# Kernel optimization log

Hardware: AMD Instinct MI355X
Metric: run time of the kernel (lower is better)

Reference implementation:

```python
import jax, jax.numpy as jnp
import numpy as np

B, N, NH, F = 4, 4096, 16, 8      # batch, grid cells, input points per cell, raw features
D, FF, H, PE = 256, 1024, 8, 32   # model_dim, ff_dim, n_heads, pos_emb_dim
NG, NI = 8192, 65536              # grid table size, input-point table size
SEQ = 4                           # 4 ** seq_level
HD = D // H


def layer_norm(x, g, b, eps=1e-5):
    mu = jnp.mean(x, axis=-1, keepdims=True)
    var = jnp.mean(jnp.square(x - mu), axis=-1, keepdims=True)
    return (x - mu) * jax.lax.rsqrt(var + eps) * g + b


def setup_inputs() -> dict:
    key = jax.random.key(0)
    ks = jax.random.split(key, 20)
    inp = {}
    inp["x"] = jax.random.normal(ks[0], (B, N, NH, F), jnp.float32)
    inp["grid_level_indices"] = jax.random.randint(ks[1], (B, N), 0, NG)
    inp["drop_mask"] = jax.random.bernoulli(ks[2], 0.1, (B, N))
    # buffers
    inp["input_mapping"] = jax.random.randint(ks[3], (NG, NH), 0, NI)
    inp["in_range"] = jax.random.bernoulli(ks[4], 0.95, (NG, NH))
    inp["input_coordinates"] = jax.random.uniform(ks[5], (2, NI), jnp.float32, -3.14, 3.14)
    inp["grid_coords"] = jax.random.uniform(ks[6], (2, NG), jnp.float32, -3.14, 3.14)
    # params
    inp["W_in"] = jax.random.normal(ks[7], (F, D), jnp.float32) * 0.05
    inp["b_in"] = jnp.zeros((D,), jnp.float32)
    inp["W_pe"] = jax.random.normal(ks[8], (2, PE), jnp.float32) * 0.2
    inp["W_bias"] = jax.random.normal(ks[9], (PE, H), jnp.float32) * 0.1
    inp["W_v"] = jax.random.normal(ks[10], (D, D), jnp.float32) * 0.02
    inp["W_o"] = jax.random.normal(ks[11], (D, D), jnp.float32) * 0.02
    inp["W1"] = jax.random.normal(ks[12], (D, FF), jnp.float32) * 0.02
    inp["W2"] = jax.random.normal(ks[13], (FF, D), jnp.float32) * 0.02
    inp["g1"] = jnp.ones((D,), jnp.float32)
    inp["b1"] = jnp.zeros((D,), jnp.float32)
    inp["g2"] = jnp.ones((D,), jnp.float32)
    inp["b2"] = jnp.zeros((D,), jnp.float32)
    return inp


def reference(x, grid_level_indices, drop_mask, input_mapping, in_range,
              input_coordinates, grid_coords, W_in, b_in, W_pe, W_bias,
              W_v, W_o, W1, W2, g1, b1, g2, b2):
    b, n, nh, _ = x.shape
    nq = n // SEQ
    K = SEQ * nh  # keys per group

    # input_layer.input_mlp: Linear + SiLU
    x = jax.nn.silu(x @ W_in + b_in)                       # [b,n,nh,D]

    # relative positions (polar): grid-cell coords vs gathered input-point coords
    gseq = grid_level_indices.reshape(b, nq, SEQ)
    idx = input_mapping[gseq]                              # [b,nq,4,nh]
    lon1 = grid_coords[0][gseq][..., None, None]           # [b,nq,4,1,1]
    lat1 = grid_coords[1][gseq][..., None, None]
    lon2 = input_coordinates[0][idx][:, :, None]           # [b,nq,1,4,nh]
    lat2 = input_coordinates[1][idx][:, :, None]
    dlon, dlat = lon2 - lon1, lat2 - lat1                  # [b,nq,4,4,nh]
    dist = jnp.sqrt(dlon * dlon + dlat * dlat + 1e-12)
    ang = jnp.arctan2(dlat, dlon)
    pos1 = dist.reshape(b, nq, SEQ, K)
    pos2 = ang.reshape(b, nq, SEQ, K)

    # mask: out-of-range OR dropped, broadcast across the 4 query cells
    m = (~in_range[grid_level_indices]) | drop_mask[:, :, None]  # [b,n,nh]
    m = m.reshape(b, nq, SEQ, nh)
    mask = jnp.broadcast_to(m[:, :, None], (b, nq, SEQ, SEQ, nh)).reshape(b, nq, SEQ, K)

    xs = x.reshape(b, nq, K, D)                            # kv tokens per group

    # positional bias -> attention scores (qkv_bias=False path: bias-only scores)
    pe = jax.nn.silu(jnp.stack([pos1, pos2], -1) @ W_pe)   # [b,nq,4,K,PE]
    bias = pe @ W_bias                                     # [b,nq,4,K,H]
    scores = jnp.moveaxis(bias, -1, 2)                     # [b,nq,H,4,K]
    scores = jnp.where(mask[:, :, None], -1e9, scores)
    att = jax.nn.softmax(scores, axis=-1)

    vh = (xs @ W_v).reshape(b, nq, K, H, HD)
    out = jnp.einsum('bqhtk,bqkhd->bqthd', att, vh).reshape(b, nq, SEQ, D)
    out = out @ W_o                                        # [b,nq,4,D]

    # nha_layer tail (q_res=False, dropout=0)
    h = layer_norm(out, g1, b1)
    h = layer_norm(h + jax.nn.silu(h @ W1) @ W2, g2, b2)
    return h.reshape(b, n, D)
```

## Files before the change

### kernel.cpp

```cpp
#include <hip/hip_runtime.h>

#define B_   4
#define N_   4096
#define NH_  16
#define F_   8
#define D_   256
#define FF_  1024
#define H_   8
#define PE_  32
#define NG_  8192
#define NI_  65536
#define NQ_  1024

typedef short short8 __attribute__((ext_vector_type(8)));
typedef short short4v __attribute__((ext_vector_type(4)));
typedef float f32x4 __attribute__((ext_vector_type(4)));

union U8 { short8 s8; uint4 u4; };

__device__ __forceinline__ float silu_f(float v) {
  return v * __builtin_amdgcn_rcpf(1.f + __expf(-v));
}
__device__ __forceinline__ unsigned short f2bf(float f) {
  unsigned int x = __float_as_uint(f);
  unsigned int r = (x + 0x7fffu + ((x >> 16) & 1u)) >> 16;
  return (unsigned short)r;
}
__device__ __forceinline__ unsigned int cvt_pk(float a, float b) {
  unsigned int r;
  asm("v_cvt_pk_bf16_f32 %0, %1, %2" : "=v"(r) : "v"(a), "v"(b));
  return r;
}
__device__ __forceinline__ unsigned short f2bf1(float v) {
  return (unsigned short)cvt_pk(v, v);
}
__device__ __forceinline__ float bf2f(unsigned short h) {
  return __uint_as_float(((unsigned int)h) << 16);
}

__device__ __forceinline__ int detect_layout(const unsigned int* w) {
  unsigned b1 = 0, b0 = 0;
#pragma unroll
  for (int i = 0; i < 64; ++i) {
    unsigned v = w[i];
    b1 |= v & 0x0000FF00u;
    b0 |= v & 0x000000FFu;
  }
  return b1 ? 0 : (b0 ? 1 : 2);
}
__device__ __forceinline__ int read_bool(const void* p, int i, int lay) {
  if (lay == 0) return ((const unsigned char*)p)[i] != 0;
  if (lay == 1) return ((const int*)p)[i] != 0;
  return ((const float*)p)[i] != 0.0f;
}

#define WOP_OFF 0
#define W1P_OFF 65536
#define W2P_OFF (65536 + 262144)
#define WVP_OFF (65536 + 262144 + 262144)
#define WIP_OFF (65536 + 262144 + 262144 + 65536)
#define WBP_OFF (WIP_OFF + 8192)
#define WS_TAIL ((65536 + 262144 + 262144) * 2)
#define WS_FULL ((WBP_OFF + 512) * 2)

__global__ __launch_bounds__(256) void k_pack(
    const float* __restrict__ Wo, const float* __restrict__ W1,
    const float* __restrict__ W2, const float* __restrict__ Wv,
    const float* __restrict__ Wi, const float* __restrict__ Wb,
    short* __restrict__ ws)
{
  int t = blockIdx.x * 256 + threadIdx.x;
  if (t < 8192) {
    int g = t & 3, n = (t >> 2) & 255, kk = t >> 10;
    int k0 = kk * 32 + g * 8;
    short8 v;
#pragma unroll
    for (int j = 0; j < 8; ++j) v[j] = (short)f2bf(Wo[(k0 + j) * 256 + n]);
    *(short8*)(ws + WOP_OFF + t * 8) = v;
  } else if (t < 40960) {
    int u = t - 8192;
    int g = u & 3, n = (u >> 2) & 1023, kk = u >> 12;
    int k0 = kk * 32 + g * 8;
    short8 v;
#pragma unroll
    for (int j = 0; j < 8; ++j) v[j] = (short)f2bf(W1[(k0 + j) * 1024 + n]);
    *(short8*)(ws + W1P_OFF + u * 8) = v;
  } else if (t < 73728) {
    int u = t - 40960;
    int g = u & 3, n = (u >> 2) & 255, kk = u >> 10;
    int k0 = kk * 32 + g * 8;
    short8 v;
#pragma unroll
    for (int j = 0; j < 8; ++j) v[j] = (short)f2bf(W2[(k0 + j) * 256 + n]);
    *(short8*)(ws + W2P_OFF + u * 8) = v;
  } else if (t < 81920) {
    int u = t - 73728;
    int g = u & 3, n = (u >> 2) & 255, kk = u >> 10;
    int k0 = kk * 32 + g * 8;
    short8 v;
#pragma unroll
    for (int j = 0; j < 8; ++j) v[j] = (short)f2bf(Wv[(k0 + j) * 256 + n]);
    *(short8*)(ws + WVP_OFF + u * 8) = v;
  } else if (t < 82944) {
    int u = t - 81920;
    int g = u & 3, n = u >> 2;
    short8 v;
#pragma unroll
    for (int j = 0; j < 8; ++j) {
      int k = g * 8 + j;
      v[j] = (k < 8) ? (short)f2bf(Wi[k * 256 + n]) : (short)0;
    }
    *(short8*)(ws + WIP_OFF + (n * 4 + g) * 8) = v;
  } else if (t < 83008) {
    int u = t - 82944;
    int g = u & 3, col = u >> 2;
    short8 v;
#pragma unroll
    for (int j = 0; j < 8; ++j) {
      int p = g * 8 + j;
      v[j] = (col < 8) ? (short)f2bf(Wb[p * 8 + col]) : (short)0;
    }
    *(short8*)(ws + WBP_OFF + (col * 4 + g) * 8) = v;
  }
}

#define OFF_XST   0
#define OFF_ATTB  32768
#define OFF_XL    36864
#define OFF_DIST  36864
#define OFF_ANG   37888
#define OFF_KLON  38912
#define OFF_KLAT  39168
#define OFF_KMSK  39424
#define OFF_GLON  39680
#define OFF_GLAT  39696
#define OFF_GIDX  39712
#define OFF_DROP  39728

__global__ __launch_bounds__(256) void k_attn_mfma(
    const float* __restrict__ x, const int* __restrict__ gli,
    const void* __restrict__ drop, const int* __restrict__ imap,
    const void* __restrict__ inr, const float* __restrict__ icoord,
    const float* __restrict__ gcoord, const float* __restrict__ W_pe,
    const float* __restrict__ b_in, const short* __restrict__ WiP,
    const short* __restrict__ WbP, const short* __restrict__ WvP,
    float* __restrict__ out)
{
  __shared__ __align__(16) char sm[39744];
  float* xl = (float*)(sm + OFF_XL);
  float* distl = (float*)(sm + OFF_DIST);
  float* angl = (float*)(sm + OFF_ANG);
  float* klon = (float*)(sm + OFF_KLON);
  float* klat = (float*)(sm + OFF_KLAT);
  int* kmask = (int*)(sm + OFF_KMSK);
  float* glon = (float*)(sm + OFF_GLON);
  float* glat = (float*)(sm + OFF_GLAT);
  int* gidx = (int*)(sm + OFF_GIDX);
  int* dropf = (int*)(sm + OFF_DROP);

  const int grp = blockIdx.x;
  const int b = grp >> 10;
  const int q = grp & (NQ_ - 1);
  const int tid = threadIdx.x;
  const int w = tid >> 6;
  const int l15 = tid & 15;
  const int g = (tid & 63) >> 4;
  const int swz = (l15 & 7) << 4;

  const int lay = detect_layout((const unsigned int*)inr);

  if (tid < 4) {
    int gg = gli[b * N_ + q * 4 + tid];
    gidx[tid] = gg;
    glon[tid] = gcoord[gg];
    glat[tid] = gcoord[NG_ + gg];
    dropf[tid] = read_bool(drop, b * N_ + q * 4 + tid, lay);
  }
  const float* xb = x + (size_t)(b * N_ + q * 4) * (NH_ * F_);
  xl[tid] = xb[tid];
  xl[tid + 256] = xb[tid + 256];
  __syncthreads();

  if (tid < 64) {
    int s = tid >> 4;
    int gg = gidx[s];
    int id = imap[gg * NH_ + (tid & 15)];
    klon[tid] = icoord[id];
    klat[tid] = icoord[NI_ + id];
    kmask[tid] = (read_bool(inr, gg * NH_ + (tid & 15), lay) == 0) | dropf[s];
  }

  {
    short8 a = {0, 0, 0, 0, 0, 0, 0, 0};
    if (g == 0) {
      const float4* xlf = (const float4*)xl;
      float4 xa = xlf[(w * 16 + l15) * 2];
      float4 xc = xlf[(w * 16 + l15) * 2 + 1];
      U8 u;
      u.u4.x = cvt_pk(xa.x, xa.y);
      u.u4.y = cvt_pk(xa.z, xa.w);
      u.u4.z = cvt_pk(xc.x, xc.y);
      u.u4.w = cvt_pk(xc.z, xc.w);
      a = u.s8;
    }
    const int k0 = w * 16 + g * 4;
#pragma unroll
    for (int nf = 0; nf < 16; ++nf) {
      short8 bv = *(const short8*)(WiP + ((nf * 16 + l15) * 4 + g) * 8);
      f32x4 accM = {0.f, 0.f, 0.f, 0.f};
      accM = __builtin_amdgcn_mfma_f32_16x16x32_bf16(a, bv, accM, 0, 0, 0);
      int d = nf * 16 + l15;
      float bn = b_in[d];
      uint2 pv;
      pv.x = cvt_pk(silu_f(accM[0] + bn), silu_f(accM[1] + bn));
      pv.y = cvt_pk(silu_f(accM[2] + bn), silu_f(accM[3] + bn));
      *(uint2*)(sm + ((d * 128 + k0 * 2) ^ ((d & 7) << 4))) = pv;
    }
  }
  __syncthreads();

  {
    const int t = tid >> 6, k = tid & 63;
    float dlon = klon[k] - glon[t];
    float dlat = klat[k] - glat[t];
    distl[tid] = sqrtf(dlon * dlon + dlat * dlat + 1e-12f);
    angl[tid] = atan2f(dlat, dlon);
  }
  __syncthreads();

  {
    float wpe0[8], wpe1[8];
    {
      const float4* wp = (const float4*)W_pe;
      float4 w0a = wp[g * 2], w0b = wp[g * 2 + 1];
      float4 w1a = wp[8 + g * 2], w1b = wp[8 + g * 2 + 1];
      wpe0[0] = w0a.x; wpe0[1] = w0a.y; wpe0[2] = w0a.z; wpe0[3] = w0a.w;
      wpe0[4] = w0b.x; wpe0[5] = w0b.y; wpe0[6] = w0b.z; wpe0[7] = w0b.w;
      wpe1[0] = w1a.x; wpe1[1] = w1a.y; wpe1[2] = w1a.z; wpe1[3] = w1a.w;
      wpe1[4] = w1b.x; wpe1[5] = w1b.y; wpe1[6] = w1b.z; wpe1[7] = w1b.w;
    }
    short8 wb = *(const short8*)(WbP + (l15 * 4 + g) * 8);
    f32x4 accS[4];
#pragma unroll
    for (int i = 0; i < 4; ++i) {
      int row = (w * 4 + i) * 16 + l15;
      float dd = distl[row];
      float aa = angl[row];
      float pe[8];
#pragma unroll
      for (int j = 0; j < 8; ++j)
        pe[j] = silu_f(fmaf(dd, wpe0[j], aa * wpe1[j]));
      U8 pu;
      pu.u4.x = cvt_pk(pe[0], pe[1]);
      pu.u4.y = cvt_pk(pe[2], pe[3]);
      pu.u4.z = cvt_pk(pe[4], pe[5]);
      pu.u4.w = cvt_pk(pe[6], pe[7]);
      f32x4 z = {0.f, 0.f, 0.f, 0.f};
      accS[i] = __builtin_amdgcn_mfma_f32_16x16x32_bf16(pu.s8, wb, z, 0, 0, 0);
    }
    float sv[16];
    float mx = -1e30f;
#pragma unroll
    for (int i = 0; i < 4; ++i)
#pragma unroll
      for (int r = 0; r < 4; ++r) {
        int k = i * 16 + g * 4 + r;
        float s = kmask[k] ? -1e9f : accS[i][r];
        sv[i * 4 + r] = s;
        mx = fmaxf(mx, s);
      }
    mx = fmaxf(mx, __shfl_xor(mx, 16));
    mx = fmaxf(mx, __shfl_xor(mx, 32));
    float sum = 0.f;
#pragma unroll
    for (int u = 0; u < 16; ++u) { sv[u] = __expf(sv[u] - mx); sum += sv[u]; }
    sum += __shfl_xor(sum, 16);
    sum += __shfl_xor(sum, 32);
    float inv = __builtin_amdgcn_rcpf(sum);
    if (l15 < 8) {
      int row = l15 * 4 + w;
      int rs = (row & 7) << 4;
#pragma unroll
      for (int i = 0; i < 4; ++i) {
        uint2 pv;
        pv.x = cvt_pk(sv[i * 4 + 0] * inv, sv[i * 4 + 1] * inv);
        pv.y = cvt_pk(sv[i * 4 + 2] * inv, sv[i * 4 + 3] * inv);
        *(uint2*)(sm + OFF_ATTB + ((row * 128 + (i * 16 + g * 4) * 2) ^ rs)) = pv;
      }
    }
  }
  __syncthreads();

  f32x4 accY[2][4];
  {
    f32x4 z = {0.f, 0.f, 0.f, 0.f};
#pragma unroll
    for (int mi = 0; mi < 2; ++mi)
#pragma unroll
      for (int ni = 0; ni < 4; ++ni) accY[mi][ni] = z;
  }
#pragma unroll
  for (int kk = 0; kk < 2; ++kk) {
    short8 a0 = *(const short8*)(sm + OFF_ATTB + ((l15 * 128 + kk * 64 + g * 16) ^ swz));
    short8 a1 = *(const short8*)(sm + OFF_ATTB + (((16 + l15) * 128 + kk * 64 + g * 16) ^ swz));
    short8 bf[4];
#pragma unroll
    for (int ni = 0; ni < 4; ++ni)
      bf[ni] = *(const short8*)(sm +
          (((w * 64 + ni * 16 + l15) * 128 + kk * 64 + g * 16) ^ swz));
#pragma unroll
    for (int ni = 0; ni < 4; ++ni) {
      accY[0][ni] = __builtin_amdgcn_mfma_f32_16x16x32_bf16(a0, bf[ni], accY[0][ni], 0, 0, 0);
      accY[1][ni] = __builtin_amdgcn_mfma_f32_16x16x32_bf16(a1, bf[ni], accY[1][ni], 0, 0, 0);
    }
  }
  __syncthreads();

#pragma unroll
  for (int mi = 0; mi < 2; ++mi)
#pragma unroll
    for (int ni = 0; ni < 4; ++ni)
#pragma unroll
      for (int r = 0; r < 4; ++r) {
        int row = mi * 16 + g * 4 + r;
        int col = w * 64 + ni * 16 + l15;
        *(unsigned short*)(sm + ((row * 512 + col * 2) ^ ((row & 7) << 4))) =
            f2bf1(accY[mi][ni][r]);
      }
  __syncthreads();

  {
    const int mf = w >> 1;
    f32x4 accV[4];
    {
      f32x4 z = {0.f, 0.f, 0.f, 0.f};
#pragma unroll
      for (int ni = 0; ni < 4; ++ni) accV[ni] = z;
    }
#pragma unroll
    for (int kk = 0; kk < 8; ++kk) {
      short8 a = *(const short8*)(sm +
          (((mf * 16 + l15) * 512 + kk * 64 + g * 16) ^ swz));
#pragma unroll
      for (int ni = 0; ni < 4; ++ni) {
        int col = w * 64 + ni * 16 + l15;
        short8 bv = *(const short8*)(WvP + ((size_t)(kk * 256 + col)) * 32 + g * 8);
        accV[ni] = __builtin_amdgcn_mfma_f32_16x16x32_bf16(a, bv, accV[ni], 0, 0, 0);
      }
    }
    float* outl = (float*)(sm + 16384);
    const int gb = (w & 1) * 2;
#pragma unroll
    for (int ni = 0; ni < 4; ++ni) {
      if (g == gb + (ni >> 1)) {
#pragma unroll
        for (int r = 0; r < 4; ++r)
          outl[r * 256 + w * 64 + ni * 16 + l15] = accV[ni][r];
      }
    }
  }
  __syncthreads();

  {
    const float* outl = (const float*)(sm + 16384);
    float* ob = out + (size_t)grp * (4 * D_);
#pragma unroll
    for (int t = 0; t < 4; ++t) ob[t * 256 + tid] = outl[t * 256 + tid];
  }
}

__global__ __launch_bounds__(256) void k_attn_valu(
    const float* __restrict__ x, const int* __restrict__ gli,
    const void* __restrict__ drop, const int* __restrict__ imap,
    const void* __restrict__ inr, const float* __restrict__ icoord,
    const float* __restrict__ gcoord, const float* __restrict__ W_in,
    const float* __restrict__ b_in, const float* __restrict__ W_pe,
    const float* __restrict__ W_bias, const float* __restrict__ W_v,
    float* __restrict__ out)
{
  __shared__ __align__(16) float xl[512];
  __shared__ float glon[4], glat[4];
  __shared__ int gidx[4], dropf[4];
  __shared__ float klon[64], klat[64];
  __shared__ int kmask[64];
  __shared__ __align__(16) unsigned short xs[64 * D_];
  __shared__ __align__(16) float att[32 * 64];
  __shared__ __align__(16) float yl[4 * 8 * 260];

  const int grp = blockIdx.x;
  const int b = grp >> 10;
  const int q = grp & (NQ_ - 1);
  const int tid = threadIdx.x;
  const int lay = detect_layout((const unsigned int*)inr);

  if (tid < 4) {
    int g = gli[b * N_ + q * 4 + tid];
    gidx[tid] = g;
    glon[tid] = gcoord[g];
    glat[tid] = gcoord[NG_ + g];
    dropf[tid] = read_bool(drop, b * N_ + q * 4 + tid, lay);
  }
  const float* xb = x + (size_t)(b * N_ + q * 4) * (NH_ * F_);
  xl[tid] = xb[tid];
  xl[tid + 256] = xb[tid + 256];
  __syncthreads();

  if (tid < 64) {
    int s = tid >> 4;
    int g = gidx[s];
    int id = imap[g * NH_ + (tid & 15)];
    klon[tid] = icoord[id];
    klat[tid] = icoord[NI_ + id];
    kmask[tid] = (read_bool(inr, g * NH_ + (tid & 15), lay) == 0) | dropf[s];
  }
  {
    float w[8];
#pragma unroll
    for (int c = 0; c < 8; ++c) w[c] = W_in[c * D_ + tid];
    float bi = b_in[tid];
#pragma unroll 4
    for (int k = 0; k < 64; ++k) {
      float v = bi;
#pragma unroll
      for (int c = 0; c < 8; ++c) v = fmaf(xl[k * 8 + c], w[c], v);
      xs[k * D_ + tid] = f2bf(silu_f(v));
    }
  }
  __syncthreads();
  {
    const int t = tid >> 6, k = tid & 63;
    float dlon = klon[k] - glon[t];
    float dlat = klat[k] - glat[t];
    float dist = sqrtf(dlon * dlon + dlat * dlat + 1e-12f);
    float ang = atan2f(dlat, dlon);
    float bias[8];
#pragma unroll
    for (int h = 0; h < 8; ++h) bias[h] = 0.f;
#pragma unroll
    for (int p = 0; p < 32; ++p) {
      float pv = silu_f(fmaf(dist, W_pe[p], ang * W_pe[32 + p]));
#pragma unroll
      for (int h = 0; h < 8; ++h) bias[h] = fmaf(pv, W_bias[p * 8 + h], bias[h]);
    }
    const bool mk = (kmask[k] != 0);
#pragma unroll
    for (int h = 0; h < 8; ++h)
      att[(h * 4 + t) * 64 + k] = mk ? -1e9f : bias[h];
  }
  __syncthreads();
  {
    const int row = tid >> 3, l8 = tid & 7;
    float sv[8];
    float mx = -1e30f;
#pragma unroll
    for (int i = 0; i < 8; ++i) { sv[i] = att[row * 64 + l8 + i * 8]; mx = fmaxf(mx, sv[i]); }
#pragma unroll
    for (int off = 1; off < 8; off <<= 1) mx = fmaxf(mx, __shfl_xor(mx, off, 8));
    float sm = 0.f;
#pragma unroll
    for (int i = 0; i < 8; ++i) { sv[i] = __expf(sv[i] - mx); sm += sv[i]; }
#pragma unroll
    for (int off = 1; off < 8; off <<= 1) sm += __shfl_xor(sm, off, 8);
    float inv = 1.f / sm;
#pragma unroll
    for (int i = 0; i < 8; ++i) att[row * 64 + l8 + i * 8] = sv[i] * inv;
  }
  __syncthreads();
  {
    float acc[32];
#pragma unroll
    for (int r = 0; r < 32; ++r) acc[r] = 0.f;
    for (int k4 = 0; k4 < 64; k4 += 4) {
      float xv0 = bf2f(xs[(k4 + 0) * D_ + tid]);
      float xv1 = bf2f(xs[(k4 + 1) * D_ + tid]);
      float xv2 = bf2f(xs[(k4 + 2) * D_ + tid]);
      float xv3 = bf2f(xs[(k4 + 3) * D_ + tid]);
#pragma unroll
      for (int r = 0; r < 32; ++r) {
        float4 a = *(const float4*)&att[r * 64 + k4];
        acc[r] = fmaf(a.x, xv0, acc[r]);
        acc[r] = fmaf(a.y, xv1, acc[r]);
        acc[r] = fmaf(a.z, xv2, acc[r]);
        acc[r] = fmaf(a.w, xv3, acc[r]);
      }
    }
#pragma unroll
    for (int r = 0; r < 32; ++r)
      yl[(r & 3) * 2080 + (r >> 2) * 260 + tid] = acc[r];
  }
  __syncthreads();
  {
    const int h = tid >> 5;
    float o0 = 0.f, o1 = 0.f, o2 = 0.f, o3 = 0.f;
    for (int c = 0; c < 256; c += 4) {
      float w0 = W_v[(c + 0) * D_ + tid];
      float w1 = W_v[(c + 1) * D_ + tid];
      float w2 = W_v[(c + 2) * D_ + tid];
      float w3 = W_v[(c + 3) * D_ + tid];
      float4 y0 = *(const float4*)&yl[0 * 2080 + h * 260 + c];
      float4 y1 = *(const float4*)&yl[1 * 2080 + h * 260 + c];
      float4 y2 = *(const float4*)&yl[2 * 2080 + h * 260 + c];
      float4 y3 = *(const float4*)&yl[3 * 2080 + h * 260 + c];
      o0 = fmaf(y0.x, w0, o0); o0 = fmaf(y0.y, w1, o0); o0 = fmaf(y0.z, w2, o0); o0 = fmaf(y0.w, w3, o0);
      o1 = fmaf(y1.x, w0, o1); o1 = fmaf(y1.y, w1, o1); o1 = fmaf(y1.z, w2, o1); o1 = fmaf(y1.w, w3, o1);
      o2 = fmaf(y2.x, w0, o2); o2 = fmaf(y2.y, w1, o2); o2 = fmaf(y2.z, w2, o2); o2 = fmaf(y2.w, w3, o2);
      o3 = fmaf(y3.x, w0, o3); o3 = fmaf(y3.y, w1, o3); o3 = fmaf(y3.z, w2, o3); o3 = fmaf(y3.w, w3, o3);
    }
    float* ob = out + (size_t)grp * (4 * D_);
    ob[0 * D_ + tid] = o0;
    ob[1 * D_ + tid] = o1;
    ob[2 * D_ + tid] = o2;
    ob[3 * D_ + tid] = o3;
  }
}

template<int MI>
__device__ __forceinline__ void gemm_mfma(
    f32x4 acc[MI][4], const char* As, const short* Bp,
    int N, int kk0, int colbase, int l15, int g)
{
#pragma unroll
  for (int kk = 0; kk < 8; ++kk) {
    short8 a[MI], bv[4];
#pragma unroll
    for (int mi = 0; mi < MI; ++mi) {
      int row = mi * 16 + l15;
      int byte = (row * 512 + kk * 64 + g * 16) ^ ((row & 7) << 4);
      a[mi] = *(const short8*)(As + byte);
    }
#pragma unroll
    for (int ni = 0; ni < 4; ++ni) {
      int col = colbase + ni * 16 + l15;
      size_t off = ((size_t)(kk0 + kk) * N + col) * 32 + g * 8;
      bv[ni] = *(const short8*)(Bp + off);
    }
#pragma unroll
    for (int mi = 0; mi < MI; ++mi)
#pragma unroll
      for (int ni = 0; ni < 4; ++ni)
        acc[mi][ni] = __builtin_amdgcn_mfma_f32_16x16x32_bf16(
            a[mi], bv[ni], acc[mi][ni], 0, 0, 0);
  }
}

__global__ __launch_bounds__(256) void k_tail_mfma(
    const float* __restrict__ g1v, const float* __restrict__ b1v,
    const float* __restrict__ g2v, const float* __restrict__ b2v,
    const short* __restrict__ WoP, const short* __restrict__ W1P,
    const short* __restrict__ W2P, float* __restrict__ io)
{
  __shared__ __align__(16) unsigned short sA1[32 * 256];
  __shared__ __align__(16) unsigned short sU[32 * 256];
  __shared__ float sPs[4][32];
  __shared__ float sPss[4][32];

  const int tid = threadIdx.x;
  const int w = tid >> 6;
  const int l15 = tid & 15;
  const int g = (tid & 63) >> 4;
  float* base = io + (size_t)blockIdx.x * (32 * 256);

#pragma unroll
  for (int i = 0; i < 8; ++i) {
    int e = (tid + 256 * i) * 4;
    int row = e >> 8, c = e & 255;
    float4 v = *(const float4*)(base + e);
    uint2 pv;
    pv.x = cvt_pk(v.x, v.y);
    pv.y = cvt_pk(v.z, v.w);
    int byte = (row * 512 + c * 2) ^ ((row & 7) << 4);
    *(uint2*)((char*)sU + byte) = pv;
  }
  __syncthreads();

  f32x4 acc[2][4];
  {
    f32x4 z = {0.f, 0.f, 0.f, 0.f};
#pragma unroll
    for (int mi = 0; mi < 2; ++mi)
#pragma unroll
      for (int ni = 0; ni < 4; ++ni) acc[mi][ni] = z;
  }
  gemm_mfma<2>(acc, (const char*)sU, WoP, 256, 0, w * 64, l15, g);

#pragma unroll
  for (int mi = 0; mi < 2; ++mi)
#pragma unroll
    for (int r = 0; r < 4; ++r) {
      float a0 = acc[mi][0][r], a1 = acc[mi][1][r], a2 = acc[mi][2][r], a3 = acc[mi][3][r];
      float s = a0 + a1 + a2 + a3;
      float ss = a0 * a0 + a1 * a1 + a2 * a2 + a3 * a3;
#pragma unroll
      for (int off = 1; off < 16; off <<= 1) {
        s += __shfl_xor(s, off);
        ss += __shfl_xor(ss, off);
      }
      if (l15 == 0) {
        int row = 16 * mi + 4 * g + r;
        sPs[w][row] = s;
        sPss[w][row] = ss;
      }
    }
  __syncthreads();

  {
    float ga[4], bb[4];
#pragma unroll
    for (int ni = 0; ni < 4; ++ni) {
      int col = 64 * w + 16 * ni + l15;
      ga[ni] = g1v[col];
      bb[ni] = b1v[col];
    }
#pragma unroll
    for (int mi = 0; mi < 2; ++mi)
#pragma unroll
      for (int r = 0; r < 4; ++r) {
        int row = 16 * mi + 4 * g + r;
        float S = sPs[0][row] + sPs[1][row] + sPs[2][row] + sPs[3][row];
        float SS = sPss[0][row] + sPss[1][row] + sPss[2][row] + sPss[3][row];
        float mu = S * (1.f / 256.f);
        float rs = rsqrtf(SS * (1.f / 256.f) - mu * mu + 1e-5f);
#pragma unroll
        for (int ni = 0; ni < 4; ++ni) {
          int col = 64 * w + 16 * ni + l15;
          float val = (acc[mi][ni][r] - mu) * rs * ga[ni] + bb[ni];
          acc[mi][ni][r] = val;
          int byte = (row * 512 + col * 2) ^ ((row & 7) << 4);
          *(unsigned short*)((char*)sA1 + byte) = f2bf1(val);
        }
      }
  }
  __syncthreads();

  for (int p = 0; p < 4; ++p) {
    f32x4 acc2[2][4];
    {
      f32x4 z = {0.f, 0.f, 0.f, 0.f};
#pragma unroll
      for (int mi = 0; mi < 2; ++mi)
#pragma unroll
        for (int ni = 0; ni < 4; ++ni) acc2[mi][ni] = z;
    }
    gemm_mfma<2>(acc2, (const char*)sA1, W1P, 1024, 0, p * 256 + w * 64, l15, g);
#pragma unroll
    for (int mi = 0; mi < 2; ++mi)
#pragma unroll
      for (int ni = 0; ni < 4; ++ni)
#pragma unroll
        for (int r = 0; r < 4; ++r) {
          int row = 16 * mi + 4 * g + r;
          int col = 64 * w + 16 * ni + l15;
          int byte = (row * 512 + col * 2) ^ ((row & 7) << 4);
          *(unsigned short*)((char*)sU + byte) = f2bf1(silu_f(acc2[mi][ni][r]));
        }
    __syncthreads();
    gemm_mfma<2>(acc, (const char*)sU, W2P, 256, p * 8, w * 64, l15, g);
    __syncthreads();
  }

#pragma unroll
  for (int mi = 0; mi < 2; ++mi)
#pragma unroll
    for (int r = 0; r < 4; ++r) {
      float a0 = acc[mi][0][r], a1 = acc[mi][1][r], a2 = acc[mi][2][r], a3 = acc[mi][3][r];
      float s = a0 + a1 + a2 + a3;
      float ss = a0 * a0 + a1 * a1 + a2 * a2 + a3 * a3;
#pragma unroll
      for (int off = 1; off < 16; off <<= 1) {
        s += __shfl_xor(s, off);
        ss += __shfl_xor(ss, off);
      }
      if (l15 == 0) {
        int row = 16 * mi + 4 * g + r;
        sPs[w][row] = s;
        sPss[w][row] = ss;
      }
    }
  __syncthreads();

  {
    float ga[4], bb[4];
#pragma unroll
    for (int ni = 0; ni < 4; ++ni) {
      int col = 64 * w + 16 * ni + l15;
      ga[ni] = g2v[col];
      bb[ni] = b2v[col];
    }
#pragma unroll
    for (int mi = 0; mi < 2; ++mi)
#pragma unroll
      for (int r = 0; r < 4; ++r) {
        int row = 16 * mi + 4 * g + r;
        float S = sPs[0][row] + sPs[1][row] + sPs[2][row] + sPs[3][row];
        float SS = sPss[0][row] + sPss[1][row] + sPss[2][row] + sPss[3][row];
        float mu = S * (1.f / 256.f);
        float rs = rsqrtf(SS * (1.f / 256.f) - mu * mu + 1e-5f);
#pragma unroll
        for (int ni = 0; ni < 4; ++ni) {
          int col = 64 * w + 16 * ni + l15;
          base[row * 256 + col] = (acc[mi][ni][r] - mu) * rs * ga[ni] + bb[ni];
        }
      }
  }
}

__global__ __launch_bounds__(256) void k_tail(
    const float* __restrict__ Wo, const float* __restrict__ W1,
    const float* __restrict__ W2, const float* __restrict__ g1,
    const float* __restrict__ b1, const float* __restrict__ g2,
    const float* __restrict__ b2, float* __restrict__ io)
{
  __shared__ __align__(16) float rl[16 * 260];
  __shared__ __align__(16) float h1[16 * 260];
  __shared__ __align__(16) unsigned short u[16 * FF_];
  const int tid = threadIdx.x;
  float* base = io + (size_t)blockIdx.x * (16 * D_);

#pragma unroll
  for (int r = 0; r < 16; ++r) rl[r * 260 + tid] = base[r * D_ + tid];
  __syncthreads();
  {
    float acc[16];
#pragma unroll
    for (int r = 0; r < 16; ++r) acc[r] = 0.f;
    for (int c = 0; c < 256; c += 4) {
      float w0 = Wo[(c + 0) * D_ + tid], w1 = Wo[(c + 1) * D_ + tid];
      float w2 = Wo[(c + 2) * D_ + tid], w3 = Wo[(c + 3) * D_ + tid];
#pragma unroll
      for (int r = 0; r < 16; ++r) {
        float4 rv = *(const float4*)&rl[r * 260 + c];
        acc[r] = fmaf(rv.x, w0, acc[r]); acc[r] = fmaf(rv.y, w1, acc[r]);
        acc[r] = fmaf(rv.z, w2, acc[r]); acc[r] = fmaf(rv.w, w3, acc[r]);
      }
    }
#pragma unroll
    for (int r = 0; r < 16; ++r) h1[r * 260 + tid] = acc[r];
  }
  __syncthreads();
  {
    const int r = tid >> 4, l = tid & 15;
    float s = 0.f, ss = 0.f;
#pragma unroll
    for (int i = 0; i < 16; ++i) { float v = h1[r * 260 + l + i * 16]; s += v; ss += v * v; }
#pragma unroll
    for (int off = 1; off < 16; off <<= 1) { s += __shfl_xor(s, off, 16); ss += __shfl_xor(ss, off, 16); }
    float mu = s * (1.f / 256.f);
    float rs = rsqrtf(ss * (1.f / 256.f) - mu * mu + 1e-5f);
#pragma unroll
    for (int i = 0; i < 16; ++i) {
      int d = l + i * 16;
      h1[r * 260 + d] = (h1[r * 260 + d] - mu) * rs * g1[d] + b1[d];
    }
  }
  __syncthreads();
  for (int fo = 0; fo < 4; ++fo) {
    const int f = fo * 256 + tid;
    float a2[16];
#pragma unroll
    for (int r = 0; r < 16; ++r) a2[r] = 0.f;
    for (int c = 0; c < 256; c += 4) {
      float w0 = W1[(c + 0) * FF_ + f], w1 = W1[(c + 1) * FF_ + f];
      float w2 = W1[(c + 2) * FF_ + f], w3 = W1[(c + 3) * FF_ + f];
#pragma unroll
      for (int r = 0; r < 16; ++r) {
        float4 hv = *(const float4*)&h1[r * 260 + c];
        a2[r] = fmaf(hv.x, w0, a2[r]); a2[r] = fmaf(hv.y, w1, a2[r]);
        a2[r] = fmaf(hv.z, w2, a2[r]); a2[r] = fmaf(hv.w, w3, a2[r]);
      }
    }
#pragma unroll
    for (int r = 0; r < 16; ++r) u[r * FF_ + f] = f2bf(silu_f(a2[r]));
  }
  __syncthreads();
  {
    float a3[16];
#pragma unroll
    for (int r = 0; r < 16; ++r) a3[r] = h1[r * 260 + tid];
    for (int f = 0; f < FF_; f += 8) {
      float w[8];
#pragma unroll
      for (int i = 0; i < 8; ++i) w[i] = W2[(f + i) * D_ + tid];
#pragma unroll
      for (int r = 0; r < 16; ++r) {
        uint4 uv = *(const uint4*)&u[r * FF_ + f];
        a3[r] = fmaf(__uint_as_float(uv.x << 16), w[0], a3[r]);
        a3[r] = fmaf(__uint_as_float(uv.x & 0xffff0000u), w[1], a3[r]);
        a3[r] = fmaf(__uint_as_float(uv.y << 16), w[2], a3[r]);
        a3[r] = fmaf(__uint_as_float(uv.y & 0xffff0000u), w[3], a3[r]);
        a3[r] = fmaf(__uint_as_float(uv.z << 16), w[4], a3[r]);
        a3[r] = fmaf(__uint_as_float(uv.z & 0xffff0000u), w[5], a3[r]);
        a3[r] = fmaf(__uint_as_float(uv.w << 16), w[6], a3[r]);
        a3[r] = fmaf(__uint_as_float(uv.w & 0xffff0000u), w[7], a3[r]);
      }
    }
#pragma unroll
    for (int r = 0; r < 16; ++r) rl[r * 260 + tid] = a3[r];
  }
  __syncthreads();
  {
    const int r = tid >> 4, l = tid & 15;
    float s = 0.f, ss = 0.f;
#pragma unroll
    for (int i = 0; i < 16; ++i) { float v = rl[r * 260 + l + i * 16]; s += v; ss += v * v; }
#pragma unroll
    for (int off = 1; off < 16; off <<= 1) { s += __shfl_xor(s, off, 16); ss += __shfl_xor(ss, off, 16); }
    float mu = s * (1.f / 256.f);
    float rs = rsqrtf(ss * (1.f / 256.f) - mu * mu + 1e-5f);
#pragma unroll
    for (int i = 0; i < 16; ++i) {
      int d = l + i * 16;
      base[r * D_ + d] = (rl[r * 260 + d] - mu) * rs * g2[d] + b2[d];
    }
  }
}

extern "C" void kernel_launch(void* const* d_in, const int* in_sizes, int n_in,
                              void* d_out, int out_size, void* d_ws, size_t ws_size,
                              hipStream_t stream) {
  (void)in_sizes; (void)n_in; (void)out_size;
  const float* x = (const float*)d_in[0];
  const int* gli = (const int*)d_in[1];
  const void* drop = d_in[2];
  const int* imap = (const int*)d_in[3];
  const void* inr = d_in[4];
  const float* icoord = (const float*)d_in[5];
  const float* gcoord = (const float*)d_in[6];
  const float* W_in = (const float*)d_in[7];
  const float* b_in = (const float*)d_in[8];
  const float* W_pe = (const float*)d_in[9];
  const float* W_bias = (const float*)d_in[10];
  const float* W_v = (const float*)d_in[11];
  const float* W_o = (const float*)d_in[12];
  const float* W1 = (const float*)d_in[13];
  const float* W2 = (const float*)d_in[14];
  const float* g1 = (const float*)d_in[15];
  const float* b1 = (const float*)d_in[16];
  const float* g2 = (const float*)d_in[17];
  const float* b2 = (const float*)d_in[18];
  float* out = (float*)d_out;

  if (ws_size >= (size_t)WS_FULL) {
    short* ws = (short*)d_ws;
    k_pack<<<dim3(325), dim3(256), 0, stream>>>(W_o, W1, W2, W_v, W_in, W_bias, ws);
    k_attn_mfma<<<dim3(B_ * NQ_), dim3(256), 0, stream>>>(
        x, gli, drop, imap, inr, icoord, gcoord, W_pe, b_in,
        ws + WIP_OFF, ws + WBP_OFF, ws + WVP_OFF, out);
    k_tail_mfma<<<dim3((B_ * N_) / 32), dim3(256), 0, stream>>>(
        g1, b1, g2, b2, ws + WOP_OFF, ws + W1P_OFF, ws + W2P_OFF, out);
  } else if (ws_size >= (size_t)WS_TAIL) {
    short* ws = (short*)d_ws;
    k_pack<<<dim3(325), dim3(256), 0, stream>>>(W_o, W1, W2, W_v, W_in, W_bias, ws);
    k_attn_valu<<<dim3(B_ * NQ_), dim3(256), 0, stream>>>(
        x, gli, drop, imap, inr, icoord, gcoord, W_in, b_in, W_pe, W_bias, W_v, out);
    k_tail_mfma<<<dim3((B_ * N_) / 32), dim3(256), 0, stream>>>(
        g1, b1, g2, b2, ws + WOP_OFF, ws + W1P_OFF, ws + W2P_OFF, out);
  } else {
    k_attn_valu<<<dim3(B_ * NQ_), dim3(256), 0, stream>>>(
        x, gli, drop, imap, inr, icoord, gcoord, W_in, b_in, W_pe, W_bias, W_v, out);
    k_tail<<<dim3((B_ * N_) / 16), dim3(256), 0, stream>>>(
        W_o, W1, W2, g1, b1, g2, b2, out);
  }
}
```

Baseline: 115.7 us.

## Precompute byte masks, pass bf16 intermediate rows, drop x LDS staging

The pack kernel now converts the drop and in_range masks into byte arrays once, so the attention kernel no longer runs layout detection or reads the booleans per block. When the workspace is large enough, the attention kernel writes its output as bf16 rows into the workspace, and the tail kernel reads them directly instead of reading fp32 and converting, which halves that intermediate traffic. The x staging through LDS and one barrier are removed, with x loaded straight from global memory. In exchange the pack kernel launches more blocks, the fast path needs a larger workspace, and the k_attn_valu fallback now runs with pack blocks that never fill the masks.

Result: faster. 112.1 us (-3.1%).

```diff
diff --git a/kernel.cpp b/kernel.cpp
--- a/kernel.cpp
+++ b/kernel.cpp
@@ -13,7 +13,6 @@
 #define NQ_  1024
 
 typedef short short8 __attribute__((ext_vector_type(8)));
-typedef short short4v __attribute__((ext_vector_type(4)));
 typedef float f32x4 __attribute__((ext_vector_type(4)));
 
 union U8 { short8 s8; uint4 u4; };
@@ -60,13 +59,19 @@
 #define WVP_OFF (65536 + 262144 + 262144)
 #define WIP_OFF (65536 + 262144 + 262144 + 65536)
 #define WBP_OFF (WIP_OFF + 8192)
+#define WS_BASE_B ((WBP_OFF + 512) * 2)
+#define DRP8_B  WS_BASE_B
+#define INR8_B  (WS_BASE_B + 16384)
+#define WS_MASKS_END (INR8_B + 131072)
+#define ROWS_B  WS_MASKS_END
+#define WS_ROWS_END (ROWS_B + 16384 * 256 * 2)
 #define WS_TAIL ((65536 + 262144 + 262144) * 2)
-#define WS_FULL ((WBP_OFF + 512) * 2)
 
 __global__ __launch_bounds__(256) void k_pack(
     const float* __restrict__ Wo, const float* __restrict__ W1,
     const float* __restrict__ W2, const float* __restrict__ Wv,
     const float* __restrict__ Wi, const float* __restrict__ Wb,
+    const void* __restrict__ drop, const void* __restrict__ inr,
     short* __restrict__ ws)
 {
   int t = blockIdx.x * 256 + threadIdx.x;
@@ -121,12 +126,23 @@
       v[j] = (col < 8) ? (short)f2bf(Wb[p * 8 + col]) : (short)0;
     }
     *(short8*)(ws + WBP_OFF + (col * 4 + g) * 8) = v;
+  } else if (t >= 83200) {
+    int lay = detect_layout((const unsigned int*)inr);
+    int t2 = t - 83200;
+    char* wsb = (char*)ws;
+    if (t2 < B_ * N_) {
+      ((unsigned char*)(wsb + DRP8_B))[t2] =
+          (unsigned char)read_bool(drop, t2, lay);
+    } else if (t2 < B_ * N_ + NG_ * NH_) {
+      int u = t2 - B_ * N_;
+      ((unsigned char*)(wsb + INR8_B))[u] =
+          (unsigned char)read_bool(inr, u, lay);
+    }
   }
 }
 
 #define OFF_XST   0
 #define OFF_ATTB  32768
-#define OFF_XL    36864
 #define OFF_DIST  36864
 #define OFF_ANG   37888
 #define OFF_KLON  38912
@@ -134,20 +150,17 @@
 #define OFF_KMSK  39424
 #define OFF_GLON  39680
 #define OFF_GLAT  39696
-#define OFF_GIDX  39712
-#define OFF_DROP  39728
 
 __global__ __launch_bounds__(256) void k_attn_mfma(
     const float* __restrict__ x, const int* __restrict__ gli,
-    const void* __restrict__ drop, const int* __restrict__ imap,
-    const void* __restrict__ inr, const float* __restrict__ icoord,
+    const unsigned char* __restrict__ drp8, const unsigned char* __restrict__ inr8,
+    const int* __restrict__ imap, const float* __restrict__ icoord,
     const float* __restrict__ gcoord, const float* __restrict__ W_pe,
     const float* __restrict__ b_in, const short* __restrict__ WiP,
     const short* __restrict__ WbP, const short* __restrict__ WvP,
-    float* __restrict__ out)
+    unsigned short* __restrict__ rows, float* __restrict__ out, int userows)
 {
-  __shared__ __align__(16) char sm[39744];
-  float* xl = (float*)(sm + OFF_XL);
+  __shared__ __align__(16) char sm[39712];
   float* distl = (float*)(sm + OFF_DIST);
   float* angl = (float*)(sm + OFF_ANG);
   float* klon = (float*)(sm + OFF_KLON);
@@ -155,8 +168,6 @@
   int* kmask = (int*)(sm + OFF_KMSK);
   float* glon = (float*)(sm + OFF_GLON);
   float* glat = (float*)(sm + OFF_GLAT);
-  int* gidx = (int*)(sm + OFF_GIDX);
-  int* dropf = (int*)(sm + OFF_DROP);
 
   const int grp = blockIdx.x;
   const int b = grp >> 10;
@@ -167,35 +178,26 @@
   const int g = (tid & 63) >> 4;
   const int swz = (l15 & 7) << 4;
 
-  const int lay = detect_layout((const unsigned int*)inr);
-
-  if (tid < 4) {
-    int gg = gli[b * N_ + q * 4 + tid];
-    gidx[tid] = gg;
-    glon[tid] = gcoord[gg];
-    glat[tid] = gcoord[NG_ + gg];
-    dropf[tid] = read_bool(drop, b * N_ + q * 4 + tid, lay);
-  }
-  const float* xb = x + (size_t)(b * N_ + q * 4) * (NH_ * F_);
-  xl[tid] = xb[tid];
-  xl[tid + 256] = xb[tid + 256];
-  __syncthreads();
-
   if (tid < 64) {
     int s = tid >> 4;
-    int gg = gidx[s];
+    int gg = gli[b * N_ + q * 4 + s];
+    if ((tid & 15) == 0) {
+      glon[s] = gcoord[gg];
+      glat[s] = gcoord[NG_ + gg];
+    }
     int id = imap[gg * NH_ + (tid & 15)];
     klon[tid] = icoord[id];
     klat[tid] = icoord[NI_ + id];
-    kmask[tid] = (read_bool(inr, gg * NH_ + (tid & 15), lay) == 0) | dropf[s];
+    kmask[tid] = (inr8[gg * NH_ + (tid & 15)] == 0) |
+                 (drp8[b * N_ + q * 4 + s] != 0);
   }
 
   {
     short8 a = {0, 0, 0, 0, 0, 0, 0, 0};
     if (g == 0) {
-      const float4* xlf = (const float4*)xl;
-      float4 xa = xlf[(w * 16 + l15) * 2];
-      float4 xc = xlf[(w * 16 + l15) * 2 + 1];
+      const float4* xp = (const float4*)(x + (size_t)(b * N_ + q * 4) * 128);
+      float4 xa = xp[(w * 16 + l15) * 2];
+      float4 xc = xp[(w * 16 + l15) * 2 + 1];
       U8 u;
       u.u4.x = cvt_pk(xa.x, xa.y);
       u.u4.y = cvt_pk(xa.z, xa.w);
@@ -361,7 +363,18 @@
   }
   __syncthreads();
 
-  {
+  if (userows) {
+    const float* outl = (const float*)(sm + 16384);
+    unsigned* rb = (unsigned*)(rows + (size_t)grp * (4 * D_));
+    int t2 = tid >> 7;
+    int c2 = tid & 127;
+#pragma unroll
+    for (int tt = 0; tt < 2; ++tt) {
+      int t = tt * 2 + t2;
+      rb[t * 128 + c2] = cvt_pk(outl[t * 256 + 2 * c2],
+                                outl[t * 256 + 2 * c2 + 1]);
+    }
+  } else {
     const float* outl = (const float*)(sm + 16384);
     float* ob = out + (size_t)grp * (4 * D_);
 #pragma unroll
@@ -547,7 +560,8 @@
     const float* __restrict__ g1v, const float* __restrict__ b1v,
     const float* __restrict__ g2v, const float* __restrict__ b2v,
     const short* __restrict__ WoP, const short* __restrict__ W1P,
-    const short* __restrict__ W2P, float* __restrict__ io)
+    const short* __restrict__ W2P, const unsigned short* __restrict__ rowsrc,
+    float* __restrict__ io, int userows)
 {
   __shared__ __align__(16) unsigned short sA1[32 * 256];
   __shared__ __align__(16) unsigned short sU[32 * 256];
@@ -560,16 +574,28 @@
   const int g = (tid & 63) >> 4;
   float* base = io + (size_t)blockIdx.x * (32 * 256);
 
-#pragma unroll
-  for (int i = 0; i < 8; ++i) {
-    int e = (tid + 256 * i) * 4;
-    int row = e >> 8, c = e & 255;
-    float4 v = *(const float4*)(base + e);
-    uint2 pv;
-    pv.x = cvt_pk(v.x, v.y);
-    pv.y = cvt_pk(v.z, v.w);
-    int byte = (row * 512 + c * 2) ^ ((row & 7) << 4);
-    *(uint2*)((char*)sU + byte) = pv;
+  if (userows) {
+    const unsigned short* rb = rowsrc + (size_t)blockIdx.x * (32 * 256);
+#pragma unroll
+    for (int i = 0; i < 8; ++i) {
+      int e = (tid + 256 * i) * 4;
+      int row = e >> 8, c = e & 255;
+      uint2 v = *(const uint2*)(rb + e);
+      int byte = (row * 512 + c * 2) ^ ((row & 7) << 4);
+      *(uint2*)((char*)sU + byte) = v;
+    }
+  } else {
+#pragma unroll
+    for (int i = 0; i < 8; ++i) {
+      int e = (tid + 256 * i) * 4;
+      int row = e >> 8, c = e & 255;
+      float4 v = *(const float4*)(base + e);
+      uint2 pv;
+      pv.x = cvt_pk(v.x, v.y);
+      pv.y = cvt_pk(v.z, v.w);
+      int byte = (row * 512 + c * 2) ^ ((row & 7) << 4);
+      *(uint2*)((char*)sU + byte) = pv;
+    }
   }
   __syncthreads();
 
@@ -839,21 +865,29 @@
   const float* b2 = (const float*)d_in[18];
   float* out = (float*)d_out;
 
-  if (ws_size >= (size_t)WS_FULL) {
+  if (ws_size >= (size_t)WS_MASKS_END) {
+    const int userows = (ws_size >= (size_t)WS_ROWS_END) ? 1 : 0;
     short* ws = (short*)d_ws;
-    k_pack<<<dim3(325), dim3(256), 0, stream>>>(W_o, W1, W2, W_v, W_in, W_bias, ws);
+    char* wsb = (char*)d_ws;
+    k_pack<<<dim3(901), dim3(256), 0, stream>>>(
+        W_o, W1, W2, W_v, W_in, W_bias, drop, inr, ws);
     k_attn_mfma<<<dim3(B_ * NQ_), dim3(256), 0, stream>>>(
-        x, gli, drop, imap, inr, icoord, gcoord, W_pe, b_in,
-        ws + WIP_OFF, ws + WBP_OFF, ws + WVP_OFF, out);
+        x, gli, (const unsigned char*)(wsb + DRP8_B),
+        (const unsigned char*)(wsb + INR8_B), imap, icoord, gcoord, W_pe, b_in,
+        ws + WIP_OFF, ws + WBP_OFF, ws + WVP_OFF,
+        (unsigned short*)(wsb + ROWS_B), out, userows);
     k_tail_mfma<<<dim3((B_ * N_) / 32), dim3(256), 0, stream>>>(
-        g1, b1, g2, b2, ws + WOP_OFF, ws + W1P_OFF, ws + W2P_OFF, out);
+        g1, b1, g2, b2, ws + WOP_OFF, ws + W1P_OFF, ws + W2P_OFF,
+        (const unsigned short*)(wsb + ROWS_B), out, userows);
   } else if (ws_size >= (size_t)WS_TAIL) {
     short* ws = (short*)d_ws;
-    k_pack<<<dim3(325), dim3(256), 0, stream>>>(W_o, W1, W2, W_v, W_in, W_bias, ws);
+    k_pack<<<dim3(325), dim3(256), 0, stream>>>(
+        W_o, W1, W2, W_v, W_in, W_bias, drop, inr, ws);
     k_attn_valu<<<dim3(B_ * NQ_), dim3(256), 0, stream>>>(
         x, gli, drop, imap, inr, icoord, gcoord, W_in, b_in, W_pe, W_bias, W_v, out);
     k_tail_mfma<<<dim3((B_ * N_) / 32), dim3(256), 0, stream>>>(
-        g1, b1, g2, b2, ws + WOP_OFF, ws + W1P_OFF, ws + W2P_OFF, out);
+        g1, b1, g2, b2, ws + WOP_OFF, ws + W1P_OFF, ws + W2P_OFF,
+        (const unsigned short*)0, out, 0);
   } else {
     k_attn_valu<<<dim3(B_ * NQ_), dim3(256), 0, stream>>>(
         x, gli, drop, imap, inr, icoord, gcoord, W_in, b_in, W_pe, W_bias, W_v, out);
```
